# Performance work log

Measured on AMD Instinct MI355X. Metric: run time of the kernel, lower is better.

## Reference

```python
import jax, jax.numpy as jnp
import numpy as np

H, W, C = 32, 32, 3
KH, KW, KC = 4, 4, 3
SHIFT = (2, 2)
K = 48
M = 200
NH, NW, NC = H // KH, W // KW, C // KC  # 8, 8, 1
NKERNEL = NH * NW * NC                  # 64
NDIM_SUB = KH * KW * KC                 # 48
NDIM = H * W * C                        # 3072
NTR = NKERNEL * K                       # 3072
N = 8192


def setup_inputs() -> dict:
    key = jax.random.key(0)
    ks = jax.random.split(key, 7)
    data = jax.random.normal(ks[0], (N, NDIM), jnp.float32)
    A_raw = jax.random.normal(ks[1], (NKERNEL, NDIM_SUB, K), jnp.float32)
    # RQspline params: knots span roughly [-5, 5]
    x0 = -5.0 + 0.1 * jax.random.normal(ks[2], (NTR, 1), jnp.float32)
    logdx = jnp.log(10.0 / (M - 1)) + 0.1 * jax.random.normal(ks[3], (NTR, M - 1), jnp.float32)
    y0 = -5.0 + 0.1 * jax.random.normal(ks[4], (NTR, 1), jnp.float32)
    logdy = jnp.log(10.0 / (M - 1)) + 0.1 * jax.random.normal(ks[5], (NTR, M - 1), jnp.float32)
    logderiv = 0.1 * jax.random.normal(ks[6], (NTR, M), jnp.float32)
    return {"data": data, "A_raw": A_raw, "x0": x0, "logdx": logdx,
            "y0": y0, "logdy": logdy, "logderiv": logderiv}


def _patch_dims():
    # Shift() is a circular roll of the flat-index image toward the origin
    dim = jnp.arange(NDIM).reshape(H, W, C)
    dim = jnp.roll(dim, shift=(-SHIFT[0], -SHIFT[1]), axis=(0, 1))
    # (NH,KH,NW,KW,C) -> (NH,NW,KH,KW,C) -> (NKERNEL, NDIM_SUB)
    return dim.reshape(NH, KH, NW, KW, C).transpose(0, 2, 1, 3, 4).reshape(NKERNEL, NDIM_SUB)


def orthogonalize(A_raw):
    # per-patch QR with sign fix, as in __init__
    Q, R = jnp.linalg.qr(A_raw)
    sign = jnp.sign(jnp.diagonal(R, axis1=-2, axis2=-1))
    return Q * sign[:, None, :]


def construct_A(A_blocks):
    rows = _patch_dims()                                               # (NKERNEL, NDIM_SUB)
    cols = K * jnp.arange(NKERNEL)[:, None] + jnp.arange(K)[None, :]   # (NKERNEL, K)
    Afull = jnp.zeros((NDIM, NTR), A_blocks.dtype)
    return Afull.at[rows[:, :, None], cols[:, None, :]].set(A_blocks)


def rqspline_forward(x, x0, logdx, y0, logdy, logderiv):
    # monotone rational-quadratic spline (Gregory-Delbourgo), per-dim knots
    xx = jnp.concatenate([x0, x0 + jnp.cumsum(jnp.exp(logdx), axis=1)], axis=1)  # (NTR, M)
    yy = jnp.concatenate([y0, y0 + jnp.cumsum(jnp.exp(logdy), axis=1)], axis=1)
    delta = jnp.exp(logderiv)
    xT = x.T                                              # (NTR, N)
    idx = jax.vmap(jnp.searchsorted)(xx, xT)              # (NTR, N)
    k = jnp.clip(idx - 1, 0, M - 2)
    xK = jnp.take_along_axis(xx, k, axis=1)
    xK1 = jnp.take_along_axis(xx, k + 1, axis=1)
    yK = jnp.take_along_axis(yy, k, axis=1)
    yK1 = jnp.take_along_axis(yy, k + 1, axis=1)
    dK = jnp.take_along_axis(delta, k, axis=1)
    dK1 = jnp.take_along_axis(delta, k + 1, axis=1)
    xi = jnp.clip((xT - xK) / (xK1 - xK), 0.0, 1.0)
    s = (yK1 - yK) / (xK1 - xK)
    xi1 = xi * (1.0 - xi)
    denom = s + (dK1 + dK - 2.0 * s) * xi1
    y_in = yK + (yK1 - yK) * (s * xi * xi + dK * xi1) / denom
    d_in = s * s * (dK1 * xi * xi + 2.0 * s * xi1 + dK * (1.0 - xi) ** 2) / (denom * denom)
    # linear extrapolation with edge derivatives outside the knot range
    below = idx == 0
    above = idx == M
    y_lo = yy[:, :1] + delta[:, :1] * (xT - xx[:, :1])
    y_hi = yy[:, -1:] + delta[:, -1:] * (xT - xx[:, -1:])
    y = jnp.where(below, y_lo, jnp.where(above, y_hi, y_in))
    d = jnp.where(below, delta[:, :1], jnp.where(above, delta[:, -1:], d_in))
    return y.T, jnp.log(d).T                              # (N, NTR) each


def reference(data, A_raw, x0, logdx, y0, logdy, logderiv):
    A = construct_A(orthogonalize(A_raw))                 # (NDIM, NTR) block-structured
    data0 = data @ A                                      # (N, NTR) patch projections
    remaining = data - data0 @ A.T
    y, logd = rqspline_forward(data0, x0, logdx, y0, logdy, logderiv)
    logj = jnp.sum(logd, axis=1)                          # (N,)
    out = remaining + y @ A.T                             # (N, NDIM)
    return out, logj
```

## Files before the change

kernel.cpp:

```cpp
#include <hip/hip_runtime.h>

#define NSMP  8192
#define NDIM  3072
#define NK    64
#define NS    48
#define MK    200
#define GB    256

__device__ __forceinline__ float rcp_fast(float x) { return __builtin_amdgcn_rcpf(x); }
__device__ __forceinline__ int imin(int a, int b) { return a < b ? a : b; }

__global__ __launch_bounds__(64) void qr_kernel(const float* __restrict__ Araw,
                                                float* __restrict__ Qws,
                                                float* __restrict__ Qpack) {
  const int k = blockIdx.x;
  const int lane = threadIdx.x;
  const float* Ak = Araw + k * NS * NS;
  float col[NS];
#pragma unroll
  for (int r = 0; r < NS; ++r)
    col[r] = (lane < NS) ? Ak[r * NS + lane] : 0.f;

  for (int j = 0; j < NS; ++j) {
    float q[NS];
#pragma unroll
    for (int r = 0; r < NS; ++r)
      q[r] = __int_as_float(__builtin_amdgcn_readlane(__float_as_int(col[r]), j));
    float n0 = 0.f, n1 = 0.f, n2 = 0.f, n3 = 0.f;
#pragma unroll
    for (int r = 0; r < NS; r += 4) {
      n0 = fmaf(q[r+0], q[r+0], n0); n1 = fmaf(q[r+1], q[r+1], n1);
      n2 = fmaf(q[r+2], q[r+2], n2); n3 = fmaf(q[r+3], q[r+3], n3);
    }
    float rinv = 1.0f / sqrtf((n0 + n1) + (n2 + n3));
#pragma unroll
    for (int r = 0; r < NS; ++r) q[r] *= rinv;
    if (lane == j) {
#pragma unroll
      for (int r = 0; r < NS; ++r) col[r] = q[r];
    } else if (lane > j && lane < NS) {
      float d0 = 0.f, d1 = 0.f, d2 = 0.f, d3 = 0.f;
#pragma unroll
      for (int r = 0; r < NS; r += 4) {
        d0 = fmaf(q[r+0], col[r+0], d0); d1 = fmaf(q[r+1], col[r+1], d1);
        d2 = fmaf(q[r+2], col[r+2], d2); d3 = fmaf(q[r+3], col[r+3], d3);
      }
      float dt = (d0 + d1) + (d2 + d3);
#pragma unroll
      for (int r = 0; r < NS; ++r) col[r] = fmaf(-dt, q[r], col[r]);
    }
  }
  if (lane < NS) {
    float* Qk = Qws + k * NS * NS;
    float* Pk = Qpack + k * NS * NS + (lane / 12) * (NS * 12) + (lane % 12);
#pragma unroll
    for (int r = 0; r < NS; ++r) {
      Qk[r * NS + lane] = col[r];
      Pk[r * 12] = col[r];
    }
  }
}

__global__ __launch_bounds__(256) void knots_kernel(
    const float* __restrict__ x0, const float* __restrict__ logdx,
    const float* __restrict__ y0, const float* __restrict__ logdy,
    const float* __restrict__ logderiv,
    float* __restrict__ xxg, float4* __restrict__ ydk8,
    float4* __restrict__ edge, unsigned char* __restrict__ gridb) {
  const int wid = threadIdx.x >> 6, lane = threadIdx.x & 63;
  const int t = blockIdx.x * 4 + wid;
  __shared__ float sxx[4][MK], syy[4][MK], sdel[4][MK];

  {
    const float* row = logdx + t * (MK - 1);
    int i0 = lane * 4;
    float e0 = (i0 + 0 < MK - 1) ? __expf(row[i0 + 0]) : 0.f;
    float e1 = (i0 + 1 < MK - 1) ? __expf(row[i0 + 1]) : 0.f;
    float e2 = (i0 + 2 < MK - 1) ? __expf(row[i0 + 2]) : 0.f;
    float e3 = (i0 + 3 < MK - 1) ? __expf(row[i0 + 3]) : 0.f;
    float p0 = e0, p1 = p0 + e1, p2 = p1 + e2, p3 = p2 + e3;
    float incl = p3;
#pragma unroll
    for (int off = 1; off < 64; off <<= 1) {
      float u = __shfl_up(incl, off, 64);
      if (lane >= off) incl += u;
    }
    float xv = x0[t];
    float base = xv + (incl - p3);
    float* xrow = xxg + t * MK;
    if (lane == 0) { xrow[0] = xv; sxx[wid][0] = xv; }
    if (i0 + 0 < MK - 1) { xrow[1+i0+0] = base + p0; sxx[wid][1+i0+0] = base + p0; }
    if (i0 + 1 < MK - 1) { xrow[1+i0+1] = base + p1; sxx[wid][1+i0+1] = base + p1; }
    if (i0 + 2 < MK - 1) { xrow[1+i0+2] = base + p2; sxx[wid][1+i0+2] = base + p2; }
    if (i0 + 3 < MK - 1) { xrow[1+i0+3] = base + p3; sxx[wid][1+i0+3] = base + p3; }
  }
  {
    const float* row = logdy + t * (MK - 1);
    int i0 = lane * 4;
    float e0 = (i0 + 0 < MK - 1) ? __expf(row[i0 + 0]) : 0.f;
    float e1 = (i0 + 1 < MK - 1) ? __expf(row[i0 + 1]) : 0.f;
    float e2 = (i0 + 2 < MK - 1) ? __expf(row[i0 + 2]) : 0.f;
    float e3 = (i0 + 3 < MK - 1) ? __expf(row[i0 + 3]) : 0.f;
    float p0 = e0, p1 = p0 + e1, p2 = p1 + e2, p3 = p2 + e3;
    float incl = p3;
#pragma unroll
    for (int off = 1; off < 64; off <<= 1) {
      float u = __shfl_up(incl, off, 64);
      if (lane >= off) incl += u;
    }
    float yv = y0[t];
    float base = yv + (incl - p3);
    if (lane == 0) syy[wid][0] = yv;
    if (i0 + 0 < MK - 1) syy[wid][1+i0+0] = base + p0;
    if (i0 + 1 < MK - 1) syy[wid][1+i0+1] = base + p1;
    if (i0 + 2 < MK - 1) syy[wid][1+i0+2] = base + p2;
    if (i0 + 3 < MK - 1) syy[wid][1+i0+3] = base + p3;
  }
  {
    const float* ld = logderiv + t * MK;
#pragma unroll
    for (int rep = 0; rep < 4; ++rep) {
      int m = lane + rep * 64;
      if (m < MK) sdel[wid][m] = __expf(ld[m]);
    }
  }
  __syncthreads();

#pragma unroll
  for (int rep = 0; rep < 4; ++rep) {
    int kk = lane + rep * 64;
    if (kk < MK - 1) {
      float xK = sxx[wid][kk], dx = sxx[wid][kk+1] - xK;
      float yK = syy[wid][kk], dy = syy[wid][kk+1] - yK;
      float rdx = 1.0f / dx;
      float s_ = dy * rdx;
      float dK = sdel[wid][kk], dK1 = sdel[wid][kk+1];
      ydk8[(t * (MK-1) + kk) * 2 + 0] = make_float4(xK, rdx, yK, dy);
      ydk8[(t * (MK-1) + kk) * 2 + 1] = make_float4(s_, dK, dK1, dK + dK1 - 2.f * s_);
    }
  }
  float xx0v = sxx[wid][0], xxMv = sxx[wid][MK-1];
  if (lane == 0) {
    float scale = (float)GB / (xxMv - xx0v);
    edge[t*2+0] = make_float4(xx0v, syy[wid][0],    sdel[wid][0],    scale);
    edge[t*2+1] = make_float4(xxMv, syy[wid][MK-1], sdel[wid][MK-1], 0.f);
  }
  float bw = (xxMv - xx0v) * (1.f / (float)GB);
#pragma unroll
  for (int i = 0; i < 4; ++i) {
    int g = lane * 4 + i;
    float L = xx0v + (float)g * bw;
    int p = 0;
#pragma unroll
    for (int st = 128; st >= 1; st >>= 1) {
      int cand = p + st;
      if (cand < MK && sxx[wid][cand] < L) p = cand;
    }
    gridb[t * GB + g] = (unsigned char)(p > MK-2 ? MK-2 : p);
  }
}

__global__ __launch_bounds__(512, 4) void core_fused(
    const float* __restrict__ data, const float* __restrict__ Qws,
    const float* __restrict__ Qpack, const float* __restrict__ xxg,
    const unsigned char* __restrict__ gridb, const float4* __restrict__ edge,
    const float4* __restrict__ ydk8, float* __restrict__ partial,
    float* __restrict__ out) {
  const int w = blockIdx.x;
  const int nh = w & 7, nw = (w >> 3) & 7, tile = w >> 6;
  const int k = nh * 8 + nw;
  const int n0 = tile * 128;
  const int tid = threadIdx.x;
  const int s = tid & 127;
  const int slice = __builtin_amdgcn_readfirstlane(tid >> 7);

  __shared__ float xs[128][49];
  __shared__ float lp[4][128];

  const int r_img = (4 * nh + slice + 2) & 31;
  const int c0 = 12 * nw + 6;

  float xreg[12];
  {
    const float* drow = data + (size_t)(n0 + s) * NDIM + r_img * 96;
#pragma unroll
    for (int e = 0; e < 6; ++e) {
      int col = c0 + 2 * e; col -= (col >= 96) ? 96 : 0;
      float2 v = *(const float2*)(drow + col);
      xreg[2*e]   = v.x; xreg[2*e+1] = v.y;
      xs[s][slice * 12 + 2*e]     = v.x;
      xs[s][slice * 12 + 2*e + 1] = v.y;
    }
  }
  __syncthreads();

  float acc[12];
#pragma unroll
  for (int j = 0; j < 12; ++j) acc[j] = 0.f;
  {
    const float4* qa = (const float4*)(Qpack + k * NS * NS + slice * (NS * 12));
#pragma unroll 4
    for (int d = 0; d < NS; ++d) {
      float xd = xs[s][d];
      float4 q0 = qa[d*3+0], q1 = qa[d*3+1], q2 = qa[d*3+2];
      acc[0] = fmaf(xd, q0.x, acc[0]); acc[1] = fmaf(xd, q0.y, acc[1]);
      acc[2] = fmaf(xd, q0.z, acc[2]); acc[3] = fmaf(xd, q0.w, acc[3]);
      acc[4] = fmaf(xd, q1.x, acc[4]); acc[5] = fmaf(xd, q1.y, acc[5]);
      acc[6] = fmaf(xd, q1.z, acc[6]); acc[7] = fmaf(xd, q1.w, acc[7]);
      acc[8] = fmaf(xd, q2.x, acc[8]); acc[9] = fmaf(xd, q2.y, acc[9]);
      acc[10]= fmaf(xd, q2.z, acc[10]); acc[11]= fmaf(xd, q2.w, acc[11]);
    }
  }

  float logsum = 0.f;
  {
    const unsigned char* gk = gridb + (size_t)k * NS * GB;
    const float4* yk = ydk8 + (size_t)k * NS * (MK - 1) * 2;
    const float4* ek = edge + (size_t)k * NS * 2;
    const float* xk = xxg + (size_t)k * NS * MK;
#pragma unroll
    for (int jj = 0; jj < 12; ++jj) {
      const int jg = slice * 12 + jj;
      float v = acc[jj];
      float4 e0 = ek[2*jg], e1 = ek[2*jg+1];
      int g = (int)((v - e0.x) * e0.w);
      g = g < 0 ? 0 : (g > GB-1 ? GB-1 : g);
      int kk = gk[jg * GB + g];
      const float* xr = xk + jg * MK;
      float xA = xr[imin(kk + 1, MK - 1)];
      float xB = xr[imin(kk + 2, MK - 1)];
      float xC = xr[imin(kk + 3, MK - 1)];
      kk += (int)(kk + 1 <= MK-2 && xA < v) + (int)(kk + 2 <= MK-2 && xB < v)
          + (int)(kk + 3 <= MK-2 && xC < v);
      float4 r0 = yk[(jg * (MK-1) + kk) * 2 + 0];
      float4 r1 = yk[(jg * (MK-1) + kk) * 2 + 1];
      float xi = (v - r0.x) * r0.y;
      xi = fminf(fmaxf(xi, 0.f), 1.f);
      float omxi = 1.f - xi, xi1 = xi * omxi, xi2 = xi * xi;
      float denom = fmaf(r1.w, xi1, r1.x);
      float rden = rcp_fast(denom);
      float y_in = fmaf(r0.w * fmaf(r1.x, xi2, r1.y * xi1), rden, r0.z);
      float d_in = r1.x * r1.x * (r1.z * xi2 + 2.f * r1.x * xi1 + r1.y * omxi * omxi) * (rden * rden);
      bool below = v <= e0.x, above = v > e1.x;
      float yv = below ? fmaf(e0.z, v - e0.x, e0.y)
               : (above ? fmaf(e1.z, v - e1.x, e1.y) : y_in);
      float dd = below ? e0.z : (above ? e1.z : d_in);
      logsum += __logf(dd);
      acc[jj] = yv - v;
    }
  }

  __syncthreads();
#pragma unroll
  for (int jj = 0; jj < 12; ++jj) xs[s][slice * 12 + jj] = acc[jj];
  __syncthreads();

  float r[12];
#pragma unroll
  for (int d = 0; d < 12; ++d) r[d] = 0.f;
  {
    const float* qc = Qws + k * NS * NS + (slice * 12) * NS;
#pragma unroll
    for (int jc = 0; jc < 12; ++jc) {
      float ea = xs[s][4*jc+0], eb = xs[s][4*jc+1];
      float ec = xs[s][4*jc+2], ed = xs[s][4*jc+3];
#pragma unroll
      for (int dd = 0; dd < 12; ++dd) {
        float4 q = *(const float4*)(qc + dd * NS + 4 * jc);
        r[dd] = fmaf(ed, q.w, fmaf(ec, q.z, fmaf(eb, q.y, fmaf(ea, q.x, r[dd]))));
      }
    }
  }

  {
    float* orow = out + (size_t)(n0 + s) * NDIM + r_img * 96;
#pragma unroll
    for (int e = 0; e < 6; ++e) {
      int col = c0 + 2 * e; col -= (col >= 96) ? 96 : 0;
      *(float2*)(orow + col) = make_float2(xreg[2*e] + r[2*e],
                                           xreg[2*e+1] + r[2*e+1]);
    }
  }

  lp[slice][s] = logsum;
  __syncthreads();
  if (tid < 128) {
    float t = lp[0][tid] + lp[1][tid] + lp[2][tid] + lp[3][tid];
    partial[(size_t)k * NSMP + n0 + tid] = t;
  }
}

__global__ __launch_bounds__(256) void reduce_kernel(const float* __restrict__ partial,
                                                     float* __restrict__ logj) {
  int n = blockIdx.x * 256 + threadIdx.x;
  float s = 0.f;
#pragma unroll
  for (int k = 0; k < NK; ++k) s += partial[k * NSMP + n];
  logj[n] = s;
}

extern "C" void kernel_launch(void* const* d_in, const int* in_sizes, int n_in,
                              void* d_out, int out_size, void* d_ws, size_t ws_size,
                              hipStream_t stream) {
  const float* data     = (const float*)d_in[0];
  const float* Araw     = (const float*)d_in[1];
  const float* x0       = (const float*)d_in[2];
  const float* logdx    = (const float*)d_in[3];
  const float* y0       = (const float*)d_in[4];
  const float* logdy    = (const float*)d_in[5];
  const float* logderiv = (const float*)d_in[6];
  float* out = (float*)d_out;
  float* ws  = (float*)d_ws;

  float*         Qws   = ws;
  float*         Qpack = Qws + 64 * NS * NS;
  float*         xxg   = Qpack + 64 * NS * NS;
  float4*        ydk8  = (float4*)(xxg + 3072 * MK);
  float4*        edge  = ydk8 + 3072 * (MK - 1) * 2;
  unsigned char* gridb = (unsigned char*)(edge + 3072 * 2);
  float*         partial = (float*)(gridb + 3072 * GB);

  qr_kernel<<<64, 64, 0, stream>>>(Araw, Qws, Qpack);
  knots_kernel<<<768, 256, 0, stream>>>(x0, logdx, y0, logdy, logderiv,
                                        xxg, ydk8, edge, gridb);
  core_fused<<<(NSMP / 128) * 64, 512, 0, stream>>>(data, Qws, Qpack, xxg,
                                                    gridb, edge, ydk8,
                                                    partial, out);
  reduce_kernel<<<32, 256, 0, stream>>>(partial, out + (size_t)NSMP * NDIM);
}
```

Before: 541.9 us.

## Shrink core blocks to 64 samples, vectorize LDS access, replace per-dim logs with product

Halves the per-block sample tile (256 threads, 64 samples) and doubles the grid, with launch bounds raised to 8 blocks per CU to improve scheduling granularity and occupancy. Shared-memory reads and writes become float2 with row pitch padded to 50, reducing LDS instruction count. The per-dimension __logf accumulation becomes a running product with one log per thread, and the logdet write is folded into an existing barrier, dropping one __syncthreads. The product of 12 derivatives could overflow or underflow for extreme values, and smaller tiles reread Q matrices more often.

```diff
diff --git a/kernel.cpp b/kernel.cpp
--- a/kernel.cpp
+++ b/kernel.cpp
@@ -160,7 +160,7 @@
   }
 }
 
-__global__ __launch_bounds__(512, 4) void core_fused(
+__global__ __launch_bounds__(256, 8) void core_fused(
     const float* __restrict__ data, const float* __restrict__ Qws,
     const float* __restrict__ Qpack, const float* __restrict__ xxg,
     const unsigned char* __restrict__ gridb, const float4* __restrict__ edge,
@@ -169,27 +169,26 @@
   const int w = blockIdx.x;
   const int nh = w & 7, nw = (w >> 3) & 7, tile = w >> 6;
   const int k = nh * 8 + nw;
-  const int n0 = tile * 128;
+  const int n0 = tile * 64;
   const int tid = threadIdx.x;
-  const int s = tid & 127;
-  const int slice = __builtin_amdgcn_readfirstlane(tid >> 7);
-
-  __shared__ float xs[128][49];
-  __shared__ float lp[4][128];
+  const int srel = tid & 63;
+  const int slice = __builtin_amdgcn_readfirstlane(tid >> 6);
+
+  __shared__ float xs[64][50];
+  __shared__ float lp[4][64];
 
   const int r_img = (4 * nh + slice + 2) & 31;
   const int c0 = 12 * nw + 6;
 
   float xreg[12];
   {
-    const float* drow = data + (size_t)(n0 + s) * NDIM + r_img * 96;
+    const float* drow = data + (size_t)(n0 + srel) * NDIM + r_img * 96;
 #pragma unroll
     for (int e = 0; e < 6; ++e) {
       int col = c0 + 2 * e; col -= (col >= 96) ? 96 : 0;
       float2 v = *(const float2*)(drow + col);
-      xreg[2*e]   = v.x; xreg[2*e+1] = v.y;
-      xs[s][slice * 12 + 2*e]     = v.x;
-      xs[s][slice * 12 + 2*e + 1] = v.y;
+      xreg[2*e] = v.x; xreg[2*e+1] = v.y;
+      *(float2*)&xs[srel][slice * 12 + 2*e] = v;
     }
   }
   __syncthreads();
@@ -200,19 +199,26 @@
   {
     const float4* qa = (const float4*)(Qpack + k * NS * NS + slice * (NS * 12));
 #pragma unroll 4
-    for (int d = 0; d < NS; ++d) {
-      float xd = xs[s][d];
-      float4 q0 = qa[d*3+0], q1 = qa[d*3+1], q2 = qa[d*3+2];
-      acc[0] = fmaf(xd, q0.x, acc[0]); acc[1] = fmaf(xd, q0.y, acc[1]);
-      acc[2] = fmaf(xd, q0.z, acc[2]); acc[3] = fmaf(xd, q0.w, acc[3]);
-      acc[4] = fmaf(xd, q1.x, acc[4]); acc[5] = fmaf(xd, q1.y, acc[5]);
-      acc[6] = fmaf(xd, q1.z, acc[6]); acc[7] = fmaf(xd, q1.w, acc[7]);
-      acc[8] = fmaf(xd, q2.x, acc[8]); acc[9] = fmaf(xd, q2.y, acc[9]);
-      acc[10]= fmaf(xd, q2.z, acc[10]); acc[11]= fmaf(xd, q2.w, acc[11]);
-    }
-  }
-
-  float logsum = 0.f;
+    for (int d2 = 0; d2 < 24; ++d2) {
+      float2 xv = *(const float2*)&xs[srel][2 * d2];
+      float4 a0 = qa[(2*d2)*3+0], a1 = qa[(2*d2)*3+1], a2 = qa[(2*d2)*3+2];
+      float4 b0 = qa[(2*d2)*3+3], b1 = qa[(2*d2)*3+4], b2 = qa[(2*d2)*3+5];
+      acc[0] = fmaf(xv.x, a0.x, acc[0]); acc[1] = fmaf(xv.x, a0.y, acc[1]);
+      acc[2] = fmaf(xv.x, a0.z, acc[2]); acc[3] = fmaf(xv.x, a0.w, acc[3]);
+      acc[4] = fmaf(xv.x, a1.x, acc[4]); acc[5] = fmaf(xv.x, a1.y, acc[5]);
+      acc[6] = fmaf(xv.x, a1.z, acc[6]); acc[7] = fmaf(xv.x, a1.w, acc[7]);
+      acc[8] = fmaf(xv.x, a2.x, acc[8]); acc[9] = fmaf(xv.x, a2.y, acc[9]);
+      acc[10]= fmaf(xv.x, a2.z, acc[10]); acc[11]= fmaf(xv.x, a2.w, acc[11]);
+      acc[0] = fmaf(xv.y, b0.x, acc[0]); acc[1] = fmaf(xv.y, b0.y, acc[1]);
+      acc[2] = fmaf(xv.y, b0.z, acc[2]); acc[3] = fmaf(xv.y, b0.w, acc[3]);
+      acc[4] = fmaf(xv.y, b1.x, acc[4]); acc[5] = fmaf(xv.y, b1.y, acc[5]);
+      acc[6] = fmaf(xv.y, b1.z, acc[6]); acc[7] = fmaf(xv.y, b1.w, acc[7]);
+      acc[8] = fmaf(xv.y, b2.x, acc[8]); acc[9] = fmaf(xv.y, b2.y, acc[9]);
+      acc[10]= fmaf(xv.y, b2.z, acc[10]); acc[11]= fmaf(xv.y, b2.w, acc[11]);
+    }
+  }
+
+  float prod = 1.f;
   {
     const unsigned char* gk = gridb + (size_t)k * NS * GB;
     const float4* yk = ydk8 + (size_t)k * NS * (MK - 1) * 2;
@@ -245,14 +251,16 @@
       float yv = below ? fmaf(e0.z, v - e0.x, e0.y)
                : (above ? fmaf(e1.z, v - e1.x, e1.y) : y_in);
       float dd = below ? e0.z : (above ? e1.z : d_in);
-      logsum += __logf(dd);
+      prod *= dd;
       acc[jj] = yv - v;
     }
   }
 
   __syncthreads();
 #pragma unroll
-  for (int jj = 0; jj < 12; ++jj) xs[s][slice * 12 + jj] = acc[jj];
+  for (int jj = 0; jj < 12; jj += 2)
+    *(float2*)&xs[srel][slice * 12 + jj] = make_float2(acc[jj], acc[jj+1]);
+  lp[slice][srel] = __logf(prod);
   __syncthreads();
 
   float r[12];
@@ -262,18 +270,18 @@
     const float* qc = Qws + k * NS * NS + (slice * 12) * NS;
 #pragma unroll
     for (int jc = 0; jc < 12; ++jc) {
-      float ea = xs[s][4*jc+0], eb = xs[s][4*jc+1];
-      float ec = xs[s][4*jc+2], ed = xs[s][4*jc+3];
+      float2 eab = *(const float2*)&xs[srel][4 * jc];
+      float2 ecd = *(const float2*)&xs[srel][4 * jc + 2];
 #pragma unroll
       for (int dd = 0; dd < 12; ++dd) {
         float4 q = *(const float4*)(qc + dd * NS + 4 * jc);
-        r[dd] = fmaf(ed, q.w, fmaf(ec, q.z, fmaf(eb, q.y, fmaf(ea, q.x, r[dd]))));
+        r[dd] = fmaf(ecd.y, q.w, fmaf(ecd.x, q.z, fmaf(eab.y, q.y, fmaf(eab.x, q.x, r[dd]))));
       }
     }
   }
 
   {
-    float* orow = out + (size_t)(n0 + s) * NDIM + r_img * 96;
+    float* orow = out + (size_t)(n0 + srel) * NDIM + r_img * 96;
 #pragma unroll
     for (int e = 0; e < 6; ++e) {
       int col = c0 + 2 * e; col -= (col >= 96) ? 96 : 0;
@@ -282,9 +290,7 @@
     }
   }
 
-  lp[slice][s] = logsum;
-  __syncthreads();
-  if (tid < 128) {
+  if (tid < 64) {
     float t = lp[0][tid] + lp[1][tid] + lp[2][tid] + lp[3][tid];
     partial[(size_t)k * NSMP + n0 + tid] = t;
   }
@@ -323,8 +329,8 @@
   qr_kernel<<<64, 64, 0, stream>>>(Araw, Qws, Qpack);
   knots_kernel<<<768, 256, 0, stream>>>(x0, logdx, y0, logdy, logderiv,
                                         xxg, ydk8, edge, gridb);
-  core_fused<<<(NSMP / 128) * 64, 512, 0, stream>>>(data, Qws, Qpack, xxg,
-                                                    gridb, edge, ydk8,
-                                                    partial, out);
+  core_fused<<<(NSMP / 64) * 64, 256, 0, stream>>>(data, Qws, Qpack, xxg,
+                                                   gridb, edge, ydk8,
+                                                   partial, out);
   reduce_kernel<<<32, 256, 0, stream>>>(partial, out + (size_t)NSMP * NDIM);
 }
```

Result: slower. 914.1 us (+68.7%).
